# Performance work log

Hardware: AMD Instinct MI355X
Metric: run time of the kernel (lower is better)

Reference implementation:

```python
import jax, jax.numpy as jnp
import numpy as np

T, A, E, RAW, H, NACT, NTP = 64, 48, 22, 512, 256, 21, 3
# entity_distinct: self entity [0], friendly entities [1:12], hostile entities [12:22]
PARAM_SHAPES = [
    ("W1", (NTP, RAW, H)), ("b1", (NTP, H)), ("W2", (NTP, H, H)), ("b2", (NTP, H)),
    ("WCf", (NTP, 2 * H, H)), ("bCf", (NTP, H)), ("WMf", (NTP, 2 * H + 2 * RAW, H)), ("bMf", (NTP, H)),
    ("WCh", (NTP, 2 * H, H)), ("bCh", (NTP, H)), ("WMh", (NTP, 2 * H + 2 * RAW, H)), ("bMh", (NTP, H)),
    ("L1", (NTP, 2 * H, H)), ("bL1", (NTP, H)), ("L2", (NTP, H, H // 2)), ("bL2", (NTP, H // 2)),
    ("L3", (NTP, H // 2, NACT)), ("bL3", (NTP, NACT)),
    ("V1", (NTP, 2 * H, H)), ("bV1", (NTP, H)), ("V2", (NTP, H, 1)), ("bV2", (NTP, 1)),
]
PNAMES = [n for n, _ in PARAM_SHAPES]


def setup_inputs() -> dict:
    key = jax.random.key(0)
    ks = jax.random.split(key, 3 + len(PARAM_SHAPES))
    inp = {
        "obs": jax.random.normal(ks[0], (T, A, E, RAW), jnp.float32),
        "hete_pick": jax.random.randint(ks[1], (T, A), 0, NTP, jnp.int32),
        "dead": jax.random.bernoulli(ks[2], 0.15, (T, A, E)),
    }
    for i, (n, s) in enumerate(PARAM_SHAPES):
        inp[n] = jax.random.normal(ks[3 + i], s, jnp.float32) * 0.02
    return inp


def _net_forward(p, obs, dead):
    relu = jax.nn.relu
    obs = jnp.where(dead[..., None], 0.0, obs)                    # nan_to_num for dead entities
    v = relu(obs @ p["W1"] + p["b1"]) @ p["W2"] + p["b2"]         # [T,A,E,H] per-entity encoder
    zs, ze_f, ze_h = obs[..., 0, :], obs[..., 1:12, :], obs[..., 12:22, :]
    vs, ve_f, ve_h = v[..., 0, :], v[..., 1:12, :], v[..., 12:22, :]
    df, dh = dead[..., 1:12], dead[..., 12:22]

    def conc(ve, d, ze, WC, bC, WM, bM):
        w = (~d).astype(obs.dtype)                                # alive mask [T,A,Ef]
        denom = jnp.maximum(w.sum(-1, keepdims=True), 1.0)
        pool = jnp.einsum('taeh,tae->tah', ve, w) / denom         # masked mean over entities
        pool_z = jnp.einsum('taer,tae->tar', ze, w) / denom       # skip-connect raw-obs pool
        vC = relu(jnp.concatenate([vs, pool], -1) @ WC + bC)
        vM = relu(jnp.concatenate([vs, pool, zs, pool_z], -1) @ WM + bM)
        return vC, vM

    vfC, vfM = conc(ve_f, df, ze_f, p["WCf"], p["bCf"], p["WMf"], p["bMf"])
    vhC, vhM = conc(ve_h, dh, ze_h, p["WCh"], p["bCh"], p["WMh"], p["bMh"])
    vC = jnp.concatenate([vfC, vhC], -1)                          # [T,A,2H] dual-conc fuse
    vM = jnp.concatenate([vfM, vhM], -1)
    logits = relu(relu(vC @ p["L1"] + p["bL1"]) @ p["L2"] + p["bL2"]) @ p["L3"] + p["bL3"]
    value = relu(vM @ p["V1"] + p["bV1"]) @ p["V2"] + p["bV2"]    # [T,A,1]
    logp = jax.nn.log_softmax(logits, -1)
    act = jnp.argmax(logits, -1)                                  # deterministic (test_mode) action
    alp = jnp.take_along_axis(logp, act[..., None], -1)           # [T,A,1] action log-prob
    return act, value, alp


def reference(obs, hete_pick, dead, W1, b1, W2, b2, WCf, bCf, WMf, bMf, WCh, bCh, WMh, bMh,
              L1, bL1, L2, bL2, L3, bL3, V1, bV1, V2, bV2):
    params = dict(W1=W1, b1=b1, W2=W2, b2=b2, WCf=WCf, bCf=bCf, WMf=WMf, bMf=bMf,
                  WCh=WCh, bCh=bCh, WMh=WMh, bMh=bMh, L1=L1, bL1=bL1, L2=L2, bL2=bL2,
                  L3=L3, bL3=bL3, V1=V1, bV1=bV1, V2=V2, bV2=bV2)
    act = jnp.zeros((T, A), jnp.int32)
    value = jnp.zeros((T, A, 1), obs.dtype)
    alp = jnp.zeros((T, A, 1), obs.dtype)
    for t in range(NTP):                                          # heterogeneous dispatch (distribute_compute)
        pt = {k: v[t] for k, v in params.items()}
        a_t, v_t, lp_t = _net_forward(pt, obs, dead)
        m = hete_pick == t                                        # mask_arr[t]
        act = jnp.where(m, a_t.astype(jnp.int32), act)
        value = jnp.where(m[..., None], v_t, value)
        alp = jnp.where(m[..., None], lp_t, alp)
    return act, value, alp
```

## Files before the change

kernel.cpp:

```cpp
#include <hip/hip_runtime.h>
#include <cstdint>

#define T_ 64
#define A_ 48
#define NP_ 3072
#define E_ 22
#define RAW_ 512
#define H_ 256
#define NACT_ 21
#define NTP_ 3
#define PV_ 3456
#define RV_ 68096
#define NDEAD_ 67584

typedef unsigned short u16;
typedef __attribute__((ext_vector_type(8))) short short8;
typedef __attribute__((ext_vector_type(4))) short short4v;
typedef __attribute__((ext_vector_type(4))) float floatx4;

__device__ __forceinline__ u16 f2bf(float x) {
    unsigned u = __float_as_uint(x);
    unsigned r = (u + 0x7FFFu + ((u >> 16) & 1u)) >> 16;
    return (u16)r;
}
__device__ __forceinline__ float bf2f(u16 h) {
    return __uint_as_float(((unsigned)h) << 16);
}

__global__ void k_bucket(const unsigned* __restrict__ deadRaw,
                         const int* __restrict__ hete, int* __restrict__ wsI)
{
    __shared__ int fl[2];
    __shared__ int sc[3], cur[3], sps[3], srs[3];
    int tid = threadIdx.x;
    if (tid < 2) fl[tid] = 0;
    if (tid < 3) { sc[tid] = 0; cur[tid] = 0; }
    __syncthreads();
    int ni = 0, nf = 0;
    for (int i = tid; i < 1024; i += 256) {
        unsigned w = deadRaw[i];
        if (w > 1u) ni = 1;
        if (w != 0u && w != 0x3F800000u) nf = 1;
    }
    if (ni) atomicOr(&fl[0], 1);
    if (nf) atomicOr(&fl[1], 1);
    for (int p = tid; p < NP_; p += 256) atomicAdd(&sc[hete[p]], 1);
    __syncthreads();
    if (tid == 0) {
        int c0 = sc[0], c1 = sc[1], c2 = sc[2];
        int p1 = (c0 + 127) & ~127;
        int p2 = p1 + ((c1 + 127) & ~127);
        sps[0] = 0; sps[1] = p1; sps[2] = p2;
        int r1 = (22 * c0 + 127) & ~127;
        int r2 = r1 + ((22 * c1 + 127) & ~127);
        srs[0] = 0; srs[1] = r1; srs[2] = r2;
        wsI[0] = fl[0] ? (fl[1] ? 2 : 1) : 0;
        wsI[1] = c0; wsI[2] = c1; wsI[3] = c2;
        wsI[4] = 0; wsI[5] = p1; wsI[6] = p2;
        wsI[8] = 0; wsI[9] = r1; wsI[10] = r2;
    }
    __syncthreads();
    int* pairIdx = wsI + 16;
    int* prb = pairIdx + PV_;
    for (int pv = tid; pv < PV_; pv += 256) pairIdx[pv] = -1;
    __syncthreads();
    for (int p = tid; p < NP_; p += 256) {
        int t = hete[p];
        int pos = atomicAdd(&cur[t], 1);
        pairIdx[sps[t] + pos] = p;
    }
    for (int pv = tid; pv < PV_; pv += 256) {
        int t = (pv >= sps[1]) + (pv >= sps[2]);
        prb[pv] = srs[t] + 22 * (pv - sps[t]);
    }
}

__global__ void k_deadmask(const void* __restrict__ dead,
                           const int* __restrict__ wsI, float* __restrict__ dm)
{
    int i = blockIdx.x * 256 + threadIdx.x;
    if (i >= NDEAD_) return;
    int mode = wsI[0];
    bool d;
    if (mode == 0)      d = ((const int*)dead)[i] != 0;
    else if (mode == 1) d = ((const float*)dead)[i] != 0.f;
    else                d = ((const unsigned char*)dead)[i] != 0;
    dm[i] = d ? 0.f : 1.f;
}

__global__ void k_rowobs(const int* __restrict__ cnt, const int* __restrict__ ps,
                         const int* __restrict__ rs, const int* __restrict__ pairIdx,
                         const float* __restrict__ dm, int* __restrict__ rowObs)
{
    int rv = blockIdx.x * 256 + threadIdx.x;
    if (rv >= RV_) return;
    int t = (rv >= rs[1]) + (rv >= rs[2]);
    int local = rv - rs[t];
    int out = -1;
    if (local < 22 * cnt[t]) {
        int pl = local / 22;
        int e = local - pl * 22;
        int p = pairIdx[ps[t] + pl];
        if (p >= 0) {
            int oi = p * 22 + e;
            if (dm[oi] != 0.f) out = oi;
        }
    }
    rowObs[rv] = out;
}

__global__ void k_wconv(const float* __restrict__ W, u16* __restrict__ Hi,
                        u16* __restrict__ Lo, int K)
{
    int K8 = K >> 3;
    int kc = blockIdx.x % K8;
    int t  = blockIdx.x / K8;
    int n  = threadIdx.x;
    const float* w = W + (long)t * K * 256 + n;
    short8 hv, lv;
#pragma unroll
    for (int j = 0; j < 8; ++j) {
        float x = w[(long)(kc * 8 + j) * 256];
        u16 hh = f2bf(x);
        hv[j] = (short)hh;
        lv[j] = (short)f2bf(x - bf2f(hh));
    }
    long o = ((long)t * 256 + n) * K + kc * 8;
    *(short8*)(Hi + o) = hv;
    *(short8*)(Lo + o) = lv;
}

#define AST 40
template<bool GATHER, bool RELU>
__global__ __launch_bounds__(256) void k_mgemm(
    const float* __restrict__ A0, const float* __restrict__ A1, int lda,
    const int* __restrict__ rowIdx,
    const u16* __restrict__ Bh0, const u16* __restrict__ Bl0,
    const u16* __restrict__ Bh1, const u16* __restrict__ Bl1,
    const float* __restrict__ bias0, const float* __restrict__ bias1,
    float* __restrict__ C0, float* __restrict__ C1, int ldc,
    int coff0, int coff1,
    const int* __restrict__ starts, int K)
{
    __shared__ short Ah[128 * AST], Al[128 * AST];
    __shared__ short Bh[128 * AST], Bl[128 * AST];

    const int tid = threadIdx.x;
    const int z = blockIdx.z;
    const float* A = z ? A1 : A0;
    const u16* Bhi = z ? Bh1 : Bh0;
    const u16* Blo = z ? Bl1 : Bl0;
    const float* bias = z ? bias1 : bias0;
    float* C = z ? C1 : C0;
    const int coff = z ? coff1 : coff0;

    const long rb = (long)blockIdx.x * 128;
    const int n0 = blockIdx.y * 128;
    const int t = (rb >= starts[0]) + (rb >= starts[1]);
    const u16* bhp = Bhi + ((long)t * 256 + n0) * K;
    const u16* blp = Blo + ((long)t * 256 + n0) * K;
    const float* biasT = bias + (long)t * 256 + n0;

    const int ar = tid >> 3;
    const int ac = (tid & 7) * 4;
    long arow[4]; float amask[4];
#pragma unroll
    for (int it = 0; it < 4; ++it) {
        int r = 32 * it + ar;
        if (GATHER) {
            int i0 = rowIdx[rb + r];
            amask[it] = (i0 < 0) ? 0.f : 1.f;
            arow[it] = (i0 < 0) ? 0 : (long)i0 * lda;
        } else {
            amask[it] = 1.f;
            arow[it] = (rb + r) * (long)lda;
        }
    }
    const int bn = tid >> 2;
    const int bc = (tid & 3) * 8;

    const int wave = tid >> 6;
    const int lane = tid & 63;
    const int wr = (wave >> 1) * 64;
    const int wc = (wave & 1) * 64;
    const int lm = lane & 15;
    const int quad = lane >> 4;

    floatx4 acc[4][4];
#pragma unroll
    for (int i = 0; i < 4; ++i)
#pragma unroll
        for (int j = 0; j < 4; ++j) acc[i][j] = (floatx4){0.f, 0.f, 0.f, 0.f};

    for (int k0 = 0; k0 < K; k0 += 32) {
        float4 av[4];
#pragma unroll
        for (int it = 0; it < 4; ++it)
            av[it] = *(const float4*)(A + arow[it] + k0 + ac);
        short8 bhv[2], blv[2];
#pragma unroll
        for (int it = 0; it < 2; ++it) {
            long off = (long)(64 * it + bn) * K + k0 + bc;
            bhv[it] = *(const short8*)(bhp + off);
            blv[it] = *(const short8*)(blp + off);
        }
        __syncthreads();
#pragma unroll
        for (int it = 0; it < 4; ++it) {
            float xs[4] = {av[it].x, av[it].y, av[it].z, av[it].w};
            short4v hv, lv;
#pragma unroll
            for (int e = 0; e < 4; ++e) {
                float x = GATHER ? xs[e] * amask[it] : xs[e];
                u16 hh = f2bf(x);
                hv[e] = (short)hh;
                lv[e] = (short)f2bf(x - bf2f(hh));
            }
            int r = 32 * it + ar;
            *(short4v*)&Ah[r * AST + ac] = hv;
            *(short4v*)&Al[r * AST + ac] = lv;
        }
#pragma unroll
        for (int it = 0; it < 2; ++it) {
            int n = 64 * it + bn;
            *(short8*)&Bh[n * AST + bc] = bhv[it];
            *(short8*)&Bl[n * AST + bc] = blv[it];
        }
        __syncthreads();
        short8 fah[4], fal[4];
#pragma unroll
        for (int i = 0; i < 4; ++i) {
            int m = wr + 16 * i + lm;
            fah[i] = *(const short8*)&Ah[m * AST + quad * 8];
            fal[i] = *(const short8*)&Al[m * AST + quad * 8];
        }
#pragma unroll
        for (int j = 0; j < 4; ++j) {
            int n = wc + 16 * j + lm;
            short8 fbh = *(const short8*)&Bh[n * AST + quad * 8];
            short8 fbl = *(const short8*)&Bl[n * AST + quad * 8];
#pragma unroll
            for (int i = 0; i < 4; ++i) {
                acc[i][j] = __builtin_amdgcn_mfma_f32_16x16x32_bf16(fah[i], fbh, acc[i][j], 0, 0, 0);
                acc[i][j] = __builtin_amdgcn_mfma_f32_16x16x32_bf16(fal[i], fbh, acc[i][j], 0, 0, 0);
                acc[i][j] = __builtin_amdgcn_mfma_f32_16x16x32_bf16(fah[i], fbl, acc[i][j], 0, 0, 0);
            }
        }
    }
#pragma unroll
    for (int j = 0; j < 4; ++j) {
        int col = wc + 16 * j + lm;
        float bj = biasT[col];
#pragma unroll
        for (int i = 0; i < 4; ++i) {
            long rbase = rb + wr + 16 * i + quad * 4;
#pragma unroll
            for (int r = 0; r < 4; ++r) {
                float vv = acc[i][j][r] + bj;
                if (RELU) vv = fmaxf(vv, 0.f);
                C[(rbase + r) * (long)ldc + coff + n0 + col] = vv;
            }
        }
    }
}

__global__ __launch_bounds__(256) void k_prep(
    const int* __restrict__ pairIdx, const int* __restrict__ prb,
    const float* __restrict__ dm, const float* __restrict__ v,
    const float* __restrict__ obs,
    float* __restrict__ XF, float* __restrict__ XH)
{
    int pv = blockIdx.x, c = threadIdx.x;
    int p = pairIdx[pv];
    float* xf = XF + (long)pv * 1536;
    float* xh = XH + (long)pv * 1536;
    if (p < 0) {
        for (int s = 0; s < 6; ++s) { xf[s * 256 + c] = 0.f; xh[s * 256 + c] = 0.f; }
        return;
    }
    __shared__ float sw[22];
    if (c < 22) sw[c] = dm[p * 22 + c];
    __syncthreads();
    float denf = 0.f, denh = 0.f;
    for (int e = 1; e < 12; ++e)  denf += sw[e];
    for (int e = 12; e < 22; ++e) denh += sw[e];
    denf = 1.f / fmaxf(denf, 1.f);
    denh = 1.f / fmaxf(denh, 1.f);

    long base = prb[pv];
    float vs = v[base * 256 + c];
    xf[c] = vs; xh[c] = vs;
    float af = 0.f, ah = 0.f;
    for (int e = 1; e < 12; ++e)  af += sw[e] * v[(base + e) * 256 + c];
    for (int e = 12; e < 22; ++e) ah += sw[e] * v[(base + e) * 256 + c];
    xf[256 + c] = af * denf;
    xh[256 + c] = ah * denh;
    const float* ob = obs + (long)p * 22 * 512;
    float w0 = sw[0];
    float z0 = ob[c] * w0;
    float z1 = ob[256 + c] * w0;
    xf[512 + c] = z0; xh[512 + c] = z0;
    xf[768 + c] = z1; xh[768 + c] = z1;
#pragma unroll
    for (int half = 0; half < 2; ++half) {
        int c2 = c + half * 256;
        float zf = 0.f, zh = 0.f;
        for (int e = 1; e < 12; ++e)  zf += sw[e] * ob[(long)e * 512 + c2];
        for (int e = 12; e < 22; ++e) zh += sw[e] * ob[(long)e * 512 + c2];
        xf[1024 + c2] = zf * denf;
        xh[1024 + c2] = zh * denh;
    }
}

__global__ __launch_bounds__(128) void k_final(
    const float* __restrict__ g1, const float* __restrict__ vV,
    const float* __restrict__ L2, const float* __restrict__ bL2,
    const float* __restrict__ L3, const float* __restrict__ bL3,
    const float* __restrict__ V2, const float* __restrict__ bV2,
    const int* __restrict__ pairIdx, const int* __restrict__ ps,
    float* __restrict__ out)
{
    int pv = blockIdx.x;
    int p = pairIdx[pv];
    if (p < 0) return;
    int c = threadIdx.x;
    int t = (pv >= ps[1]) + (pv >= ps[2]);

    __shared__ float sg1[256], sg2[128], sval[2];
    const float* g1p = g1 + (long)pv * 256;
    sg1[c] = g1p[c];
    sg1[c + 128] = g1p[c + 128];

    const float* vv = vV + (long)pv * 256;
    const float* v2t = V2 + t * 256;
    float s = vv[c] * v2t[c] + vv[c + 128] * v2t[c + 128];
    for (int off = 32; off; off >>= 1) s += __shfl_down(s, off);
    if ((c & 63) == 0) sval[c >> 6] = s;
    __syncthreads();

    const float* l2 = L2 + (long)t * 256 * 128 + c;
    float a = bL2[t * 128 + c];
#pragma unroll 8
    for (int k = 0; k < 256; ++k) a = fmaf(sg1[k], l2[(long)k * 128], a);
    sg2[c] = fmaxf(a, 0.f);
    __syncthreads();

    if (c < 64) {
        float lg = -3.0e38f;
        if (c < 21) {
            const float* l3t = L3 + (long)t * 128 * 21 + c;
            float acc = bL3[t * 21 + c];
            for (int k = 0; k < 128; ++k) acc = fmaf(sg2[k], l3t[k * 21], acc);
            lg = acc;
        }
        float mv = lg; int mi = (c < 21) ? c : 9999;
        for (int off = 32; off; off >>= 1) {
            float ov = __shfl_down(mv, off);
            int oi = __shfl_down(mi, off);
            if (ov > mv || (ov == mv && oi < mi)) { mv = ov; mi = oi; }
        }
        mv = __shfl(mv, 0); mi = __shfl(mi, 0);
        float e = (c < 21) ? expf(lg - mv) : 0.f;
        for (int off = 32; off; off >>= 1) e += __shfl_down(e, off);
        if (c == 0) {
            out[p] = (float)mi;
            out[NP_ + p] = sval[0] + sval[1] + bV2[t];
            out[2 * NP_ + p] = -logf(e);
        }
    }
}

extern "C" void kernel_launch(void* const* d_in, const int* in_sizes, int n_in,
                              void* d_out, int out_size, void* d_ws, size_t ws_size,
                              hipStream_t stream)
{
    const float* obs = (const float*)d_in[0];
    const int* hete = (const int*)d_in[1];
    const void* dead = d_in[2];
    const float* W1 = (const float*)d_in[3];  const float* b1 = (const float*)d_in[4];
    const float* W2 = (const float*)d_in[5];  const float* b2 = (const float*)d_in[6];
    const float* WCf = (const float*)d_in[7]; const float* bCf = (const float*)d_in[8];
    const float* WMf = (const float*)d_in[9]; const float* bMf = (const float*)d_in[10];
    const float* WCh = (const float*)d_in[11]; const float* bCh = (const float*)d_in[12];
    const float* WMh = (const float*)d_in[13]; const float* bMh = (const float*)d_in[14];
    const float* L1 = (const float*)d_in[15]; const float* bL1 = (const float*)d_in[16];
    const float* L2 = (const float*)d_in[17]; const float* bL2 = (const float*)d_in[18];
    const float* L3 = (const float*)d_in[19]; const float* bL3 = (const float*)d_in[20];
    const float* V1 = (const float*)d_in[21]; const float* bV1 = (const float*)d_in[22];
    const float* V2 = (const float*)d_in[23]; const float* bV2 = (const float*)d_in[24];
    float* out = (float*)d_out;

    int* wsI = (int*)d_ws;
    int* pairIdx = wsI + 16;
    int* prb = pairIdx + PV_;
    int* rowObs = prb + PV_;
    long fbase = ((16L + PV_ + PV_ + RV_) + 63) & ~63L;
    float* wsF = (float*)d_ws;
    float* dm = wsF + fbase;
    float* cur = dm + NDEAD_;
    auto allocUS = [&](long K) { u16* p = (u16*)cur; cur += (3L * 256 * K) / 2; return p; };
    u16* W1h = allocUS(512);  u16* W1l = allocUS(512);
    u16* W2h = allocUS(256);  u16* W2l = allocUS(256);
    u16* WCfh = allocUS(512); u16* WCfl = allocUS(512);
    u16* WChh = allocUS(512); u16* WChl = allocUS(512);
    u16* WMfh = allocUS(1536); u16* WMfl = allocUS(1536);
    u16* WMhh = allocUS(1536); u16* WMhl = allocUS(1536);
    u16* L1h = allocUS(512);  u16* L1l = allocUS(512);
    u16* V1h = allocUS(512);  u16* V1l = allocUS(512);
    float* regA = cur;
    float* regB = regA + (long)RV_ * 256;
    float* h1 = regA;
    float* XF = regA;
    float* XH = XF + (long)PV_ * 1536;
    float* v = regB;
    float* vC = regB;
    float* vM = vC + (long)PV_ * 512;
    float* g1 = vM + (long)PV_ * 512;
    float* vV = g1 + (long)PV_ * 256;

    k_bucket<<<1, 256, 0, stream>>>((const unsigned*)dead, hete, wsI);
    k_deadmask<<<264, 256, 0, stream>>>(dead, wsI, dm);
    k_rowobs<<<266, 256, 0, stream>>>(wsI + 1, wsI + 4, wsI + 8, pairIdx, dm, rowObs);

    k_wconv<<<3 * 512 / 8, 256, 0, stream>>>(W1, W1h, W1l, 512);
    k_wconv<<<3 * 256 / 8, 256, 0, stream>>>(W2, W2h, W2l, 256);
    k_wconv<<<3 * 512 / 8, 256, 0, stream>>>(WCf, WCfh, WCfl, 512);
    k_wconv<<<3 * 512 / 8, 256, 0, stream>>>(WCh, WChh, WChl, 512);
    k_wconv<<<3 * 1536 / 8, 256, 0, stream>>>(WMf, WMfh, WMfl, 1536);
    k_wconv<<<3 * 1536 / 8, 256, 0, stream>>>(WMh, WMhh, WMhl, 1536);
    k_wconv<<<3 * 512 / 8, 256, 0, stream>>>(L1, L1h, L1l, 512);
    k_wconv<<<3 * 512 / 8, 256, 0, stream>>>(V1, V1h, V1l, 512);

    k_mgemm<true, true><<<dim3(RV_ / 128, 2, 1), 256, 0, stream>>>(
        obs, obs, 512, rowObs, W1h, W1l, W1h, W1l, b1, b1,
        h1, h1, 256, 0, 0, wsI + 9, 512);
    k_mgemm<false, false><<<dim3(RV_ / 128, 2, 1), 256, 0, stream>>>(
        h1, h1, 256, nullptr, W2h, W2l, W2h, W2l, b2, b2,
        v, v, 256, 0, 0, wsI + 9, 256);

    k_prep<<<PV_, 256, 0, stream>>>(pairIdx, prb, dm, v, obs, XF, XH);

    k_mgemm<false, true><<<dim3(PV_ / 128, 2, 2), 256, 0, stream>>>(
        XF, XH, 1536, nullptr, WCfh, WCfl, WChh, WChl, bCf, bCh,
        vC, vC, 512, 0, 256, wsI + 5, 512);
    k_mgemm<false, true><<<dim3(PV_ / 128, 2, 2), 256, 0, stream>>>(
        XF, XH, 1536, nullptr, WMfh, WMfl, WMhh, WMhl, bMf, bMh,
        vM, vM, 512, 0, 256, wsI + 5, 1536);
    k_mgemm<false, true><<<dim3(PV_ / 128, 2, 2), 256, 0, stream>>>(
        vC, vM, 512, nullptr, L1h, L1l, V1h, V1l, bL1, bV1,
        g1, vV, 256, 0, 0, wsI + 5, 512);

    k_final<<<PV_, 128, 0, stream>>>(g1, vV, L2, bL2, L3, bL3, V2, bV2,
                                     pairIdx, wsI + 4, out);
    (void)in_sizes; (void)n_in; (void)out_size; (void)ws_size;
}
```

Before: 614.3 us.

## Store activations pre-split into packed bf16 hi/lo and read B fragments directly

Intermediate activations (h1, prep outputs, vC, vM) are written as packed hi/lo bf16 pairs in one u32, so downstream GEMMs skip the per-tile fp32-to-bf16 split and just unpack. B-operand fragments are loaded straight from global memory into registers instead of being staged through shared memory. This halves LDS usage and removes B staging stores. The cost is uncoalesced, strided global loads for B that lean on the cache.

Result: slower. 728.3 us (+18.6%).

```diff
diff --git a/kernel.cpp b/kernel.cpp
--- a/kernel.cpp
+++ b/kernel.cpp
@@ -14,6 +14,7 @@
 #define NDEAD_ 67584
 
 typedef unsigned short u16;
+typedef unsigned int u32;
 typedef __attribute__((ext_vector_type(8))) short short8;
 typedef __attribute__((ext_vector_type(4))) short short4v;
 typedef __attribute__((ext_vector_type(4))) float floatx4;
@@ -25,6 +26,11 @@
 }
 __device__ __forceinline__ float bf2f(u16 h) {
     return __uint_as_float(((unsigned)h) << 16);
+}
+__device__ __forceinline__ u32 packsplit(float x) {
+    u16 h = f2bf(x);
+    u16 l = f2bf(x - bf2f(h));
+    return (((u32)h) << 16) | l;
 }
 
 __global__ void k_bucket(const unsigned* __restrict__ deadRaw,
@@ -131,27 +137,25 @@
 }
 
 #define AST 40
-template<bool GATHER, bool RELU>
+template<int AMODE, bool RELU, bool OUTSPLIT>
 __global__ __launch_bounds__(256) void k_mgemm(
-    const float* __restrict__ A0, const float* __restrict__ A1, int lda,
+    const void* __restrict__ A0v, const void* __restrict__ A1v, int lda,
     const int* __restrict__ rowIdx,
     const u16* __restrict__ Bh0, const u16* __restrict__ Bl0,
     const u16* __restrict__ Bh1, const u16* __restrict__ Bl1,
     const float* __restrict__ bias0, const float* __restrict__ bias1,
-    float* __restrict__ C0, float* __restrict__ C1, int ldc,
+    void* __restrict__ C0v, void* __restrict__ C1v, int ldc,
     int coff0, int coff1,
     const int* __restrict__ starts, int K)
 {
     __shared__ short Ah[128 * AST], Al[128 * AST];
-    __shared__ short Bh[128 * AST], Bl[128 * AST];
 
     const int tid = threadIdx.x;
     const int z = blockIdx.z;
-    const float* A = z ? A1 : A0;
+    const void* Av = z ? A1v : A0v;
     const u16* Bhi = z ? Bh1 : Bh0;
     const u16* Blo = z ? Bl1 : Bl0;
     const float* bias = z ? bias1 : bias0;
-    float* C = z ? C1 : C0;
     const int coff = z ? coff1 : coff0;
 
     const long rb = (long)blockIdx.x * 128;
@@ -161,23 +165,24 @@
     const u16* blp = Blo + ((long)t * 256 + n0) * K;
     const float* biasT = bias + (long)t * 256 + n0;
 
-    const int ar = tid >> 3;
-    const int ac = (tid & 7) * 4;
+    const int ar0 = tid >> 3;
+    const int ac0 = (tid & 7) * 4;
+    const int ar1 = tid >> 2;
+    const int ac1 = (tid & 3) * 8;
     long arow[4]; float amask[4];
-#pragma unroll
-    for (int it = 0; it < 4; ++it) {
-        int r = 32 * it + ar;
-        if (GATHER) {
+    if (AMODE == 0) {
+#pragma unroll
+        for (int it = 0; it < 4; ++it) {
+            int r = 32 * it + ar0;
             int i0 = rowIdx[rb + r];
             amask[it] = (i0 < 0) ? 0.f : 1.f;
             arow[it] = (i0 < 0) ? 0 : (long)i0 * lda;
-        } else {
-            amask[it] = 1.f;
-            arow[it] = (rb + r) * (long)lda;
-        }
-    }
-    const int bn = tid >> 2;
-    const int bc = (tid & 3) * 8;
+        }
+    } else {
+#pragma unroll
+        for (int it = 0; it < 2; ++it)
+            arow[it] = (rb + 64 * it + ar1) * (long)lda;
+    }
 
     const int wave = tid >> 6;
     const int lane = tid & 63;
@@ -185,6 +190,8 @@
     const int wc = (wave & 1) * 64;
     const int lm = lane & 15;
     const int quad = lane >> 4;
+    const u16* bwh = bhp + (long)(wc + lm) * K + quad * 8;
+    const u16* bwl = blp + (long)(wc + lm) * K + quad * 8;
 
     floatx4 acc[4][4];
 #pragma unroll
@@ -193,40 +200,61 @@
         for (int j = 0; j < 4; ++j) acc[i][j] = (floatx4){0.f, 0.f, 0.f, 0.f};
 
     for (int k0 = 0; k0 < K; k0 += 32) {
-        float4 av[4];
-#pragma unroll
-        for (int it = 0; it < 4; ++it)
-            av[it] = *(const float4*)(A + arow[it] + k0 + ac);
-        short8 bhv[2], blv[2];
-#pragma unroll
-        for (int it = 0; it < 2; ++it) {
-            long off = (long)(64 * it + bn) * K + k0 + bc;
-            bhv[it] = *(const short8*)(bhp + off);
-            blv[it] = *(const short8*)(blp + off);
+        if (AMODE == 0) {
+            const float* A = (const float*)Av;
+            float4 av[4];
+#pragma unroll
+            for (int it = 0; it < 4; ++it)
+                av[it] = *(const float4*)(A + arow[it] + k0 + ac0);
+            __syncthreads();
+#pragma unroll
+            for (int it = 0; it < 4; ++it) {
+                float xs[4] = {av[it].x, av[it].y, av[it].z, av[it].w};
+                short4v hv, lv;
+#pragma unroll
+                for (int e = 0; e < 4; ++e) {
+                    float x = xs[e] * amask[it];
+                    u16 hh = f2bf(x);
+                    hv[e] = (short)hh;
+                    lv[e] = (short)f2bf(x - bf2f(hh));
+                }
+                int r = 32 * it + ar0;
+                *(short4v*)&Ah[r * AST + ac0] = hv;
+                *(short4v*)&Al[r * AST + ac0] = lv;
+            }
+        } else {
+            const u32* A = (const u32*)Av;
+            uint4 u0[2], u1[2];
+#pragma unroll
+            for (int it = 0; it < 2; ++it) {
+                u0[it] = *(const uint4*)(A + arow[it] + k0 + ac1);
+                u1[it] = *(const uint4*)(A + arow[it] + k0 + ac1 + 4);
+            }
+            __syncthreads();
+#pragma unroll
+            for (int it = 0; it < 2; ++it) {
+                u32 w[8] = {u0[it].x, u0[it].y, u0[it].z, u0[it].w,
+                            u1[it].x, u1[it].y, u1[it].z, u1[it].w};
+                short8 hv, lv;
+#pragma unroll
+                for (int e = 0; e < 8; ++e) {
+                    hv[e] = (short)(w[e] >> 16);
+                    lv[e] = (short)(w[e] & 0xFFFFu);
+                }
+                int r = 64 * it + ar1;
+                *(short8*)&Ah[r * AST + ac1] = hv;
+                *(short8*)&Al[r * AST + ac1] = lv;
+            }
         }
         __syncthreads();
-#pragma unroll
-        for (int it = 0; it < 4; ++it) {
-            float xs[4] = {av[it].x, av[it].y, av[it].z, av[it].w};
-            short4v hv, lv;
-#pragma unroll
-            for (int e = 0; e < 4; ++e) {
-                float x = GATHER ? xs[e] * amask[it] : xs[e];
-                u16 hh = f2bf(x);
-                hv[e] = (short)hh;
-                lv[e] = (short)f2bf(x - bf2f(hh));
-            }
-            int r = 32 * it + ar;
-            *(short4v*)&Ah[r * AST + ac] = hv;
-            *(short4v*)&Al[r * AST + ac] = lv;
-        }
-#pragma unroll
-        for (int it = 0; it < 2; ++it) {
-            int n = 64 * it + bn;
-            *(short8*)&Bh[n * AST + bc] = bhv[it];
-            *(short8*)&Bl[n * AST + bc] = blv[it];
-        }
-        __syncthreads();
+
+        short8 fbh[4], fbl[4];
+#pragma unroll
+        for (int j = 0; j < 4; ++j) {
+            long o = (long)(16 * j) * K + k0;
+            fbh[j] = *(const short8*)(bwh + o);
+            fbl[j] = *(const short8*)(bwl + o);
+        }
         short8 fah[4], fal[4];
 #pragma unroll
         for (int i = 0; i < 4; ++i) {
@@ -236,14 +264,11 @@
         }
 #pragma unroll
         for (int j = 0; j < 4; ++j) {
-            int n = wc + 16 * j + lm;
-            short8 fbh = *(const short8*)&Bh[n * AST + quad * 8];
-            short8 fbl = *(const short8*)&Bl[n * AST + quad * 8];
 #pragma unroll
             for (int i = 0; i < 4; ++i) {
-                acc[i][j] = __builtin_amdgcn_mfma_f32_16x16x32_bf16(fah[i], fbh, acc[i][j], 0, 0, 0);
-                acc[i][j] = __builtin_amdgcn_mfma_f32_16x16x32_bf16(fal[i], fbh, acc[i][j], 0, 0, 0);
-                acc[i][j] = __builtin_amdgcn_mfma_f32_16x16x32_bf16(fah[i], fbl, acc[i][j], 0, 0, 0);
+                acc[i][j] = __builtin_amdgcn_mfma_f32_16x16x32_bf16(fah[i], fbh[j], acc[i][j], 0, 0, 0);
+                acc[i][j] = __builtin_amdgcn_mfma_f32_16x16x32_bf16(fal[i], fbh[j], acc[i][j], 0, 0, 0);
+                acc[i][j] = __builtin_amdgcn_mfma_f32_16x16x32_bf16(fah[i], fbl[j], acc[i][j], 0, 0, 0);
             }
         }
     }
@@ -258,7 +283,9 @@
             for (int r = 0; r < 4; ++r) {
                 float vv = acc[i][j][r] + bj;
                 if (RELU) vv = fmaxf(vv, 0.f);
-                C[(rbase + r) * (long)ldc + coff + n0 + col] = vv;
+                long o = (rbase + r) * (long)ldc + coff + n0 + col;
+                if (OUTSPLIT) ((u32*)(z ? C1v : C0v))[o] = packsplit(vv);
+                else          ((float*)(z ? C1v : C0v))[o] = vv;
             }
         }
     }
@@ -268,14 +295,14 @@
     const int* __restrict__ pairIdx, const int* __restrict__ prb,
     const float* __restrict__ dm, const float* __restrict__ v,
     const float* __restrict__ obs,
-    float* __restrict__ XF, float* __restrict__ XH)
+    u32* __restrict__ XF, u32* __restrict__ XH)
 {
     int pv = blockIdx.x, c = threadIdx.x;
     int p = pairIdx[pv];
-    float* xf = XF + (long)pv * 1536;
-    float* xh = XH + (long)pv * 1536;
+    u32* xf = XF + (long)pv * 1536;
+    u32* xh = XH + (long)pv * 1536;
     if (p < 0) {
-        for (int s = 0; s < 6; ++s) { xf[s * 256 + c] = 0.f; xh[s * 256 + c] = 0.f; }
+        for (int s = 0; s < 6; ++s) { xf[s * 256 + c] = 0u; xh[s * 256 + c] = 0u; }
         return;
     }
     __shared__ float sw[22];
@@ -288,17 +315,17 @@
     denh = 1.f / fmaxf(denh, 1.f);
 
     long base = prb[pv];
-    float vs = v[base * 256 + c];
+    u32 vs = packsplit(v[base * 256 + c]);
     xf[c] = vs; xh[c] = vs;
     float af = 0.f, ah = 0.f;
     for (int e = 1; e < 12; ++e)  af += sw[e] * v[(base + e) * 256 + c];
     for (int e = 12; e < 22; ++e) ah += sw[e] * v[(base + e) * 256 + c];
-    xf[256 + c] = af * denf;
-    xh[256 + c] = ah * denh;
+    xf[256 + c] = packsplit(af * denf);
+    xh[256 + c] = packsplit(ah * denh);
     const float* ob = obs + (long)p * 22 * 512;
     float w0 = sw[0];
-    float z0 = ob[c] * w0;
-    float z1 = ob[256 + c] * w0;
+    u32 z0 = packsplit(ob[c] * w0);
+    u32 z1 = packsplit(ob[256 + c] * w0);
     xf[512 + c] = z0; xh[512 + c] = z0;
     xf[768 + c] = z1; xh[768 + c] = z1;
 #pragma unroll
@@ -307,8 +334,8 @@
         float zf = 0.f, zh = 0.f;
         for (int e = 1; e < 12; ++e)  zf += sw[e] * ob[(long)e * 512 + c2];
         for (int e = 12; e < 22; ++e) zh += sw[e] * ob[(long)e * 512 + c2];
-        xf[1024 + c2] = zf * denf;
-        xh[1024 + c2] = zh * denh;
+        xf[1024 + c2] = packsplit(zf * denf);
+        xh[1024 + c2] = packsplit(zh * denh);
     }
 }
 
@@ -409,13 +436,13 @@
     u16* V1h = allocUS(512);  u16* V1l = allocUS(512);
     float* regA = cur;
     float* regB = regA + (long)RV_ * 256;
-    float* h1 = regA;
-    float* XF = regA;
-    float* XH = XF + (long)PV_ * 1536;
+    u32* h1p = (u32*)regA;
+    u32* XFp = (u32*)regA;
+    u32* XHp = XFp + (long)PV_ * 1536;
     float* v = regB;
-    float* vC = regB;
-    float* vM = vC + (long)PV_ * 512;
-    float* g1 = vM + (long)PV_ * 512;
+    u32* vCp = (u32*)regB;
+    u32* vMp = vCp + (long)PV_ * 512;
+    float* g1 = (float*)(vMp + (long)PV_ * 512);
     float* vV = g1 + (long)PV_ * 256;
 
     k_bucket<<<1, 256, 0, stream>>>((const unsigned*)dead, hete, wsI);
@@ -431,23 +458,23 @@
     k_wconv<<<3 * 512 / 8, 256, 0, stream>>>(L1, L1h, L1l, 512);
     k_wconv<<<3 * 512 / 8, 256, 0, stream>>>(V1, V1h, V1l, 512);
 
-    k_mgemm<true, true><<<dim3(RV_ / 128, 2, 1), 256, 0, stream>>>(
+    k_mgemm<0, true, true><<<dim3(RV_ / 128, 2, 1), 256, 0, stream>>>(
         obs, obs, 512, rowObs, W1h, W1l, W1h, W1l, b1, b1,
-        h1, h1, 256, 0, 0, wsI + 9, 512);
-    k_mgemm<false, false><<<dim3(RV_ / 128, 2, 1), 256, 0, stream>>>(
-        h1, h1, 256, nullptr, W2h, W2l, W2h, W2l, b2, b2,
+        h1p, h1p, 256, 0, 0, wsI + 9, 512);
+    k_mgemm<1, false, false><<<dim3(RV_ / 128, 2, 1), 256, 0, stream>>>(
+        h1p, h1p, 256, nullptr, W2h, W2l, W2h, W2l, b2, b2,
         v, v, 256, 0, 0, wsI + 9, 256);
 
-    k_prep<<<PV_, 256, 0, stream>>>(pairIdx, prb, dm, v, obs, XF, XH);
-
-    k_mgemm<false, true><<<dim3(PV_ / 128, 2, 2), 256, 0, stream>>>(
-        XF, XH, 1536, nullptr, WCfh, WCfl, WChh, WChl, bCf, bCh,
-        vC, vC, 512, 0, 256, wsI + 5, 512);
-    k_mgemm<false, true><<<dim3(PV_ / 128, 2, 2), 256, 0, stream>>>(
-        XF, XH, 1536, nullptr, WMfh, WMfl, WMhh, WMhl, bMf, bMh,
-        vM, vM, 512, 0, 256, wsI + 5, 1536);
-    k_mgemm<false, true><<<dim3(PV_ / 128, 2, 2), 256, 0, stream>>>(
-        vC, vM, 512, nullptr, L1h, L1l, V1h, V1l, bL1, bV1,
+    k_prep<<<PV_, 256, 0, stream>>>(pairIdx, prb, dm, v, obs, XFp, XHp);
+
+    k_mgemm<1, true, true><<<dim3(PV_ / 128, 2, 2), 256, 0, stream>>>(
+        XFp, XHp, 1536, nullptr, WCfh, WCfl, WChh, WChl, bCf, bCh,
+        vCp, vCp, 512, 0, 256, wsI + 5, 512);
+    k_mgemm<1, true, true><<<dim3(PV_ / 128, 2, 2), 256, 0, stream>>>(
+        XFp, XHp, 1536, nullptr, WMfh, WMfl, WMhh, WMhl, bMf, bMh,
+        vMp, vMp, 512, 0, 256, wsI + 5, 1536);
+    k_mgemm<1, true, false><<<dim3(PV_ / 128, 2, 2), 256, 0, stream>>>(
+        vCp, vMp, 512, nullptr, L1h, L1l, V1h, V1l, bL1, bV1,
         g1, vV, 256, 0, 0, wsI + 5, 512);
 
     k_final<<<PV_, 128, 0, stream>>>(g1, vV, L2, bL2, L3, bL3, V2, bV2,
```
